# Performance work log

Measured on AMD Instinct MI355X. Metric: run time of the kernel, lower is better.

## Reference

```python
import jax, jax.numpy as jnp
import numpy as np

jax.config.update("jax_enable_x64", True)

L_MAX = 9  # matches init_kwargs; K = (L_MAX+1)**2 = 100 modes
SQRT_2_OVER_PI = float(np.sqrt(2.0 / np.pi))


def _l_array(l_max):
    # l repeated 2l+1 times (one entry per (l, m) mode), as float like torch.Tensor
    ls = np.concatenate([np.full(2 * i + 1, i) for i in range(l_max + 1)])
    return jnp.asarray(ls, dtype=jnp.float64)


def _bessel_up(r, k, l_arr, l_max):
    x = r.astype(jnp.float64)[..., None] * k.astype(jnp.float64)  # [N, K]
    j0 = jnp.sin(x) / x
    y = jnp.where(l_arr == 0, j0, 0.0)
    j1 = j0 / x - jnp.cos(x) / x
    y = jnp.where(l_arr == 1, j1, y)
    for i in range(1, l_max):  # small static loop over l (l_max-1 iters)
        j2 = (2 * i + 1) / x * j1 - j0
        y = jnp.where(l_arr == i + 1, j2, y)
        j0, j1 = j1, j2
    y = jnp.where(jnp.abs(x) < 1e-30, 0.0, y)
    y = y * SQRT_2_OVER_PI * k.astype(jnp.float64)
    return y.astype(jnp.float32)


def _bessel_down(r, k, l_arr, l_max):
    x = r.astype(jnp.float64)[..., None] * k.astype(jnp.float64)  # [N, K]
    y = jnp.zeros_like(x)
    lstart = l_max + int(np.sqrt(10 * l_max))
    j2 = jnp.zeros_like(x)
    j1 = jnp.ones_like(x)
    j0 = j1
    for i in range(lstart, 0, -1):  # small static downward recurrence
        j0 = (2 * i + 1) / x * j1 - j2
        if i - 1 < l_max + 1:
            y = jnp.where(l_arr == (i - 1), j0, y)
        j2, j1 = j1, j0
    true_j0 = jnp.sinc(x / jnp.pi)  # = sin(x)/x, matches torch.sinc(r/pi)
    y = y / j0 * true_j0
    small = x < 1e-20
    y = jnp.where(small & (l_arr > 0), 0.0, y)
    y = jnp.where(small & (l_arr == 0), 1.0, y)
    y = y * SQRT_2_OVER_PI * k.astype(jnp.float64)
    return y.astype(jnp.float32)


def setup_inputs() -> dict:
    key = jax.random.key(0)
    k1, k2 = jax.random.split(key)
    N = 262144
    K = (L_MAX + 1) ** 2  # 100
    r = jax.random.uniform(k1, (N,), dtype=jnp.float32, minval=0.1, maxval=20.0)
    k = jax.random.uniform(k2, (K,), dtype=jnp.float32, minval=0.5, maxval=5.0)
    return {"r": r, "k": k}


def reference(r, k):
    l_arr = _l_array(L_MAX)
    up = _bessel_up(r, k, l_arr, L_MAX)    # [N, K] f32
    dn = _bessel_down(r, k, l_arr, L_MAX)  # [N, K] f32
    x32 = r[..., None] * k                 # f32, like the torch forward
    return jnp.where(x32 < l_arr.astype(jnp.float32), dn, up)
```

## Files before the change

kernel.cpp:

```cpp
#include <hip/hip_runtime.h>
#include <math.h>


static constexpr int KMODES = 100;
static constexpr int NTILE  = 64;
static constexpr int LSTRIDE = 101;
static constexpr float S2PI = 0.79788456080286536f;

__device__ __forceinline__ float rcpf(float x) { return __builtin_amdgcn_rcpf(x); }

template<int L> struct CFc;
template<> struct CFc<2>{ static constexpr float sg[2]={3.f,-1.f};                                      static constexpr float gm[1]={-3.f}; };
template<> struct CFc<3>{ static constexpr float sg[2]={15.f,-6.f};                                     static constexpr float gm[2]={-15.f,1.f}; };
template<> struct CFc<4>{ static constexpr float sg[3]={105.f,-45.f,1.f};                               static constexpr float gm[2]={-105.f,10.f}; };
template<> struct CFc<5>{ static constexpr float sg[3]={945.f,-420.f,15.f};                             static constexpr float gm[3]={-945.f,105.f,-1.f}; };
template<> struct CFc<6>{ static constexpr float sg[4]={10395.f,-4725.f,210.f,-1.f};                    static constexpr float gm[3]={-10395.f,1260.f,-21.f}; };
template<> struct CFc<7>{ static constexpr float sg[4]={135135.f,-62370.f,3150.f,-28.f};                static constexpr float gm[4]={-135135.f,17325.f,-378.f,1.f}; };
template<> struct CFc<8>{ static constexpr float sg[5]={2027025.f,-945945.f,51975.f,-630.f,1.f};        static constexpr float gm[4]={-2027025.f,270270.f,-6930.f,36.f}; };
template<> struct CFc<9>{ static constexpr float sg[5]={34459425.f,-16216200.f,945945.f,-13860.f,45.f}; static constexpr float gm[5]={-34459425.f,4729725.f,-135135.f,990.f,-1.f}; };

__device__ __constant__ const float XCUT[10] =
  {0.f, 0.f, 0.088f, 0.29f, 0.61f, 1.01f, 1.48f, 2.00f, 2.55f, 3.14f};

template<int N>
__device__ __forceinline__ float polyH(float z, const float (&a)[N]) {
  float h = a[0];
#pragma unroll
  for (int i = 1; i < N; ++i) h = fmaf(h, z, a[i]);
  return h;
}

template<int L>
__device__ __forceinline__ void do_l(float rv, const float* __restrict__ kvec,
                                     float* ldsrow) {
#pragma unroll
  for (int m = 0; m < 2 * L + 1; ++m) {
    const int KK = L * L + m;
    float kv = kvec[KK];
    float x  = rv * kv;
    float res;
    if constexpr (L == 0) {
      res = __sinf(x) * rcpf(x);
    } else {
      float u = rcpf(x);
      float s, c;
      __sincosf(x, &s, &c);
      float z = u * u;
      if constexpr (L == 1) {
        res = fmaf(s, z, -(c * u));
      } else {
        float sv = polyH(z, CFc<L>::sg);
        float gv = polyH(z, CFc<L>::gm);
        if constexpr (L & 1) res = fmaf(s * z, sv, (c * u) * gv);
        else                 res = fmaf(s * u, sv, (c * z) * gv);
        res = (x < XCUT[L]) ? 0.0f : res;
      }
    }
    ldsrow[KK] = res * (S2PI * kv);
  }
}

__global__ __launch_bounds__(256) void sbf_kernel(const float* __restrict__ r,
                                                  const float* __restrict__ kvec,
                                                  float* __restrict__ out) {
  __shared__ float lds[NTILE * LSTRIDE];
  int tid = threadIdx.x;
  int w = tid >> 6, lane = tid & 63;
  int n0 = blockIdx.x * NTILE;
  float rv = r[n0 + lane];
  float* ldsrow = &lds[lane * LSTRIDE];
  if (w == 0)      { do_l<9>(rv, kvec, ldsrow); do_l<2>(rv, kvec, ldsrow); }
  else if (w == 1) { do_l<8>(rv, kvec, ldsrow); do_l<3>(rv, kvec, ldsrow); }
  else if (w == 2) { do_l<7>(rv, kvec, ldsrow); do_l<4>(rv, kvec, ldsrow); do_l<0>(rv, kvec, ldsrow); }
  else             { do_l<6>(rv, kvec, ldsrow); do_l<5>(rv, kvec, ldsrow); do_l<1>(rv, kvec, ldsrow); }
  __syncthreads();
  size_t base = (size_t)n0 * KMODES;
#pragma unroll
  for (int it = 0; it < 7; ++it) {
    int e = it * 1024 + tid * 4;
    if (e < NTILE * KMODES) {
      int row = (int)((unsigned)e / 100u);
      int col = e - row * 100;
      int a = row * LSTRIDE + col;
      float4 v = make_float4(lds[a], lds[a + 1], lds[a + 2], lds[a + 3]);
      *reinterpret_cast<float4*>(&out[base + e]) = v;
    }
  }
}

extern "C" void kernel_launch(void* const* d_in, const int* in_sizes, int n_in,
                              void* d_out, int out_size, void* d_ws, size_t ws_size,
                              hipStream_t stream) {
  const float* r = (const float*)d_in[0];
  const float* k = (const float*)d_in[1];
  float* out = (float*)d_out;
  int N = in_sizes[0];
  int blocks = N / NTILE;
  sbf_kernel<<<blocks, 256, 0, stream>>>(r, k, out);
}
```

Baseline: 24.48 us.

## Process two tiles per block and fold sqrt(2/pi) into polynomial coefficients

```diff
diff --git a/kernel.cpp b/kernel.cpp
--- a/kernel.cpp
+++ b/kernel.cpp
@@ -2,25 +2,32 @@
 #include <math.h>
 
 
-static constexpr int KMODES = 100;
-static constexpr int NTILE  = 64;
+static constexpr int KMODES  = 100;
+static constexpr int NTILE   = 64;
 static constexpr int LSTRIDE = 101;
-static constexpr float S2PI = 0.79788456080286536f;
+static constexpr int TPB     = 2;
+static constexpr float S2PI  = 0.79788456080286536f;
 
 __device__ __forceinline__ float rcpf(float x) { return __builtin_amdgcn_rcpf(x); }
 
 template<int L> struct CFc;
-template<> struct CFc<2>{ static constexpr float sg[2]={3.f,-1.f};                                      static constexpr float gm[1]={-3.f}; };
-template<> struct CFc<3>{ static constexpr float sg[2]={15.f,-6.f};                                     static constexpr float gm[2]={-15.f,1.f}; };
-template<> struct CFc<4>{ static constexpr float sg[3]={105.f,-45.f,1.f};                               static constexpr float gm[2]={-105.f,10.f}; };
-template<> struct CFc<5>{ static constexpr float sg[3]={945.f,-420.f,15.f};                             static constexpr float gm[3]={-945.f,105.f,-1.f}; };
-template<> struct CFc<6>{ static constexpr float sg[4]={10395.f,-4725.f,210.f,-1.f};                    static constexpr float gm[3]={-10395.f,1260.f,-21.f}; };
-template<> struct CFc<7>{ static constexpr float sg[4]={135135.f,-62370.f,3150.f,-28.f};                static constexpr float gm[4]={-135135.f,17325.f,-378.f,1.f}; };
-template<> struct CFc<8>{ static constexpr float sg[5]={2027025.f,-945945.f,51975.f,-630.f,1.f};        static constexpr float gm[4]={-2027025.f,270270.f,-6930.f,36.f}; };
-template<> struct CFc<9>{ static constexpr float sg[5]={34459425.f,-16216200.f,945945.f,-13860.f,45.f}; static constexpr float gm[5]={-34459425.f,4729725.f,-135135.f,990.f,-1.f}; };
+template<> struct CFc<2>{ static constexpr float sg[2]={S2PI*3.f,S2PI*-1.f};                         static constexpr float gm[1]={S2PI*-3.f}; };
+template<> struct CFc<3>{ static constexpr float sg[2]={S2PI*15.f,S2PI*-6.f};                        static constexpr float gm[2]={S2PI*-15.f,S2PI*1.f}; };
+template<> struct CFc<4>{ static constexpr float sg[3]={S2PI*105.f,S2PI*-45.f,S2PI*1.f};             static constexpr float gm[2]={S2PI*-105.f,S2PI*10.f}; };
+template<> struct CFc<5>{ static constexpr float sg[3]={S2PI*945.f,S2PI*-420.f,S2PI*15.f};           static constexpr float gm[3]={S2PI*-945.f,S2PI*105.f,S2PI*-1.f}; };
+template<> struct CFc<6>{ static constexpr float sg[4]={S2PI*10395.f,S2PI*-4725.f,S2PI*210.f,S2PI*-1.f};
+                          static constexpr float gm[3]={S2PI*-10395.f,S2PI*1260.f,S2PI*-21.f}; };
+template<> struct CFc<7>{ static constexpr float sg[4]={S2PI*135135.f,S2PI*-62370.f,S2PI*3150.f,S2PI*-28.f};
+                          static constexpr float gm[4]={S2PI*-135135.f,S2PI*17325.f,S2PI*-378.f,S2PI*1.f}; };
+template<> struct CFc<8>{ static constexpr float sg[5]={S2PI*2027025.f,S2PI*-945945.f,S2PI*51975.f,S2PI*-630.f,S2PI*1.f};
+                          static constexpr float gm[4]={S2PI*-2027025.f,S2PI*270270.f,S2PI*-6930.f,S2PI*36.f}; };
+template<> struct CFc<9>{ static constexpr float sg[5]={S2PI*34459425.f,S2PI*-16216200.f,S2PI*945945.f,S2PI*-13860.f,S2PI*45.f};
+                          static constexpr float gm[5]={S2PI*-34459425.f,S2PI*4729725.f,S2PI*-135135.f,S2PI*990.f,S2PI*-1.f}; };
 
-__device__ __constant__ const float XCUT[10] =
-  {0.f, 0.f, 0.088f, 0.29f, 0.61f, 1.01f, 1.48f, 2.00f, 2.55f, 3.14f};
+template<int L> __device__ __forceinline__ constexpr float xcut() {
+  constexpr float t[10] = {0.f,0.f,0.088f,0.29f,0.61f,1.01f,1.48f,2.00f,2.55f,3.14f};
+  return t[L];
+}
 
 template<int N>
 __device__ __forceinline__ float polyH(float z, const float (&a)[N]) {
@@ -40,23 +47,22 @@
     float x  = rv * kv;
     float res;
     if constexpr (L == 0) {
-      res = __sinf(x) * rcpf(x);
+      res = (__sinf(x) * rcpf(x)) * S2PI;
     } else {
+      float s = __sinf(x), c = __cosf(x);
       float u = rcpf(x);
-      float s, c;
-      __sincosf(x, &s, &c);
       float z = u * u;
       if constexpr (L == 1) {
-        res = fmaf(s, z, -(c * u));
+        res = fmaf(s, z, -(c * u)) * S2PI;
       } else {
         float sv = polyH(z, CFc<L>::sg);
         float gv = polyH(z, CFc<L>::gm);
         if constexpr (L & 1) res = fmaf(s * z, sv, (c * u) * gv);
         else                 res = fmaf(s * u, sv, (c * z) * gv);
-        res = (x < XCUT[L]) ? 0.0f : res;
+        res = (x < xcut<L>()) ? 0.0f : res;
       }
     }
-    ldsrow[KK] = res * (S2PI * kv);
+    ldsrow[KK] = res * kv;
   }
 }
 
@@ -64,26 +70,40 @@
                                                   const float* __restrict__ kvec,
                                                   float* __restrict__ out) {
   __shared__ float lds[NTILE * LSTRIDE];
-  int tid = threadIdx.x;
-  int w = tid >> 6, lane = tid & 63;
-  int n0 = blockIdx.x * NTILE;
-  float rv = r[n0 + lane];
+  const int tid = threadIdx.x;
+  const int w = tid >> 6, lane = tid & 63;
   float* ldsrow = &lds[lane * LSTRIDE];
-  if (w == 0)      { do_l<9>(rv, kvec, ldsrow); do_l<2>(rv, kvec, ldsrow); }
-  else if (w == 1) { do_l<8>(rv, kvec, ldsrow); do_l<3>(rv, kvec, ldsrow); }
-  else if (w == 2) { do_l<7>(rv, kvec, ldsrow); do_l<4>(rv, kvec, ldsrow); do_l<0>(rv, kvec, ldsrow); }
-  else             { do_l<6>(rv, kvec, ldsrow); do_l<5>(rv, kvec, ldsrow); do_l<1>(rv, kvec, ldsrow); }
-  __syncthreads();
-  size_t base = (size_t)n0 * KMODES;
+
+  float rva[TPB];
 #pragma unroll
-  for (int it = 0; it < 7; ++it) {
-    int e = it * 1024 + tid * 4;
-    if (e < NTILE * KMODES) {
-      int row = (int)((unsigned)e / 100u);
-      int col = e - row * 100;
-      int a = row * LSTRIDE + col;
-      float4 v = make_float4(lds[a], lds[a + 1], lds[a + 2], lds[a + 3]);
-      *reinterpret_cast<float4*>(&out[base + e]) = v;
+  for (int t = 0; t < TPB; ++t)
+    rva[t] = r[(blockIdx.x + t * gridDim.x) * NTILE + lane];
+
+#pragma unroll
+  for (int t = 0; t < TPB; ++t) {
+    const int tile = blockIdx.x + t * (int)gridDim.x;
+    const float rv = rva[t];
+    if (t > 0) {
+      asm volatile("s_waitcnt lgkmcnt(0)" ::: "memory");
+      __builtin_amdgcn_s_barrier();
+    }
+    if (w == 0)      { do_l<9>(rv, kvec, ldsrow); do_l<2>(rv, kvec, ldsrow); }
+    else if (w == 1) { do_l<8>(rv, kvec, ldsrow); do_l<3>(rv, kvec, ldsrow); }
+    else if (w == 2) { do_l<7>(rv, kvec, ldsrow); do_l<4>(rv, kvec, ldsrow); do_l<0>(rv, kvec, ldsrow); }
+    else             { do_l<6>(rv, kvec, ldsrow); do_l<5>(rv, kvec, ldsrow); do_l<1>(rv, kvec, ldsrow); }
+    asm volatile("s_waitcnt lgkmcnt(0)" ::: "memory");
+    __builtin_amdgcn_s_barrier();
+    size_t base = (size_t)tile * (size_t)(NTILE * KMODES);
+#pragma unroll
+    for (int it = 0; it < 7; ++it) {
+      int e = it * 1024 + tid * 4;
+      if (e < NTILE * KMODES) {
+        int row = (int)((unsigned)e / 100u);
+        int col = e - row * 100;
+        int a = row * LSTRIDE + col;
+        float4 v = make_float4(lds[a], lds[a + 1], lds[a + 2], lds[a + 3]);
+        *reinterpret_cast<float4*>(&out[base + e]) = v;
+      }
     }
   }
 }
@@ -95,6 +115,6 @@
   const float* k = (const float*)d_in[1];
   float* out = (float*)d_out;
   int N = in_sizes[0];
-  int blocks = N / NTILE;
+  int blocks = N / NTILE / TPB;
   sbf_kernel<<<blocks, 256, 0, stream>>>(r, k, out);
 }
```

Result: slower. 25.14 us (+2.7%).
